# Performance work log

Measured on AMD Instinct MI355X. Metric: run time of the kernel, lower is better.

The kernel has to match this reference:

```python
import jax, jax.numpy as jnp
import numpy as np

D_MODEL = 1024
D_STATE = 64
BATCH = 16
SEQ = 4096


def setup_inputs() -> dict:
    key = jax.random.key(0)
    ks = jax.random.split(key, 4)
    x = jax.random.normal(ks[0], (BATCH, SEQ, D_MODEL), dtype=jnp.float32)
    A = jax.random.normal(ks[1], (D_STATE, D_STATE), dtype=jnp.float32) * 0.01
    B_mat = jax.random.normal(ks[2], (D_STATE, D_MODEL), dtype=jnp.float32) * 0.01
    C = jax.random.normal(ks[3], (D_MODEL, D_STATE), dtype=jnp.float32) * 0.01
    gamma = jnp.ones((D_MODEL,), dtype=jnp.float32)
    beta = jnp.zeros((D_MODEL,), dtype=jnp.float32)
    return {"x": x, "A": A, "B_mat": B_mat, "C": C, "gamma": gamma, "beta": beta}


def reference(x, A, B_mat, C, gamma, beta):
    # x: [B, L, D]; linear SSM recurrence: s_t = s_{t-1} A^T + u_t B^T, y_t = s_t C^T
    Bsz = x.shape[0]
    xu = jnp.einsum('bld,sd->lbs', x, B_mat)  # precompute input projection [L, B, S]

    def step(state, u_t):
        state = state @ A.T + u_t          # [B, S]
        return state, state

    init = jnp.zeros((Bsz, D_STATE), dtype=x.dtype)
    _, states = jax.lax.scan(step, init, xu)   # [L, B, S]
    y = jnp.einsum('lbs,ds->bld', states, C)   # [B, L, D]

    act = jax.nn.gelu(y, approximate=False)    # torch nn.GELU default = exact
    mean = jnp.mean(act, axis=-1, keepdims=True)
    var = jnp.var(act, axis=-1, keepdims=True)
    normed = (act - mean) * jax.lax.rsqrt(var + 1e-5) * gamma + beta
    return jnp.nan_to_num(normed, nan=0.0, posinf=1e6, neginf=-1e6)
```

## Files before the change

### kernel.cpp

```cpp
#include <hip/hip_runtime.h>
#include <hip/hip_bf16.h>
#include <math.h>

#define BSZ  16
#define LSEQ 4096
#define DM   1024
#define DS   64
#define CHK  64
#define NCHK 64
#define FK   12
#define FIXT 8

typedef __bf16 bf16;
typedef bf16  bf16x8 __attribute__((ext_vector_type(8)));
typedef bf16  bf16x4 __attribute__((ext_vector_type(4)));
typedef float f32x4  __attribute__((ext_vector_type(4)));

#define MFMA(a,b,c) __builtin_amdgcn_mfma_f32_16x16x32_bf16((a),(b),(c),0,0,0)

__global__ __launch_bounds__(256) void k_prep(const float* __restrict__ Bm,
                                              const float* __restrict__ Cm,
                                              bf16* __restrict__ Bh,
                                              bf16* __restrict__ Ch) {
    int i = blockIdx.x * 256 + threadIdx.x;
    Bh[i] = (bf16)Bm[i];
    Ch[i] = (bf16)Cm[i];
}

__global__ __launch_bounds__(1024) void k_apow(const float* __restrict__ A,
                                               bf16* __restrict__ Apow) {
    __shared__ float P0[64 * 64], P1[64 * 64];
    const int tid = threadIdx.x;
    const int i = tid >> 4, j4 = (tid & 15) * 4;

    #pragma unroll
    for (int q = 0; q < 4; ++q) {
        int j = j4 + q;
        Apow[i * 64 + j] = (bf16)((i == j) ? 1.f : 0.f);
        P0[i * 64 + j]   = A[i * 64 + j];
    }
    __syncthreads();

    float* cur = P0; float* nxt = P1;
    for (int k = 1; k < FK; ++k) {
        const float4 v = *(const float4*)&cur[i * 64 + j4];
        Apow[k * 4096 + i * 64 + j4 + 0] = (bf16)v.x;
        Apow[k * 4096 + i * 64 + j4 + 1] = (bf16)v.y;
        Apow[k * 4096 + i * 64 + j4 + 2] = (bf16)v.z;
        Apow[k * 4096 + i * 64 + j4 + 3] = (bf16)v.w;
        float a0 = 0.f, a1 = 0.f, a2 = 0.f, a3 = 0.f;
        for (int m = 0; m < 64; ++m) {
            const float am = A[i * 64 + m];
            const float4 cr = *(const float4*)&cur[m * 64 + j4];
            a0 = fmaf(am, cr.x, a0);
            a1 = fmaf(am, cr.y, a1);
            a2 = fmaf(am, cr.z, a2);
            a3 = fmaf(am, cr.w, a3);
        }
        __syncthreads();
        nxt[i * 64 + j4 + 0] = a0;
        nxt[i * 64 + j4 + 1] = a1;
        nxt[i * 64 + j4 + 2] = a2;
        nxt[i * 64 + j4 + 3] = a3;
        __syncthreads();
        float* t = cur; cur = nxt; nxt = t;
    }
}

__global__ __launch_bounds__(256) void k_fir(const float* __restrict__ x,
                                             const bf16* __restrict__ Bh,
                                             const bf16* __restrict__ Apow,
                                             bf16* __restrict__ states) {
    const int c = blockIdx.x, b = blockIdx.y;
    const int tid = threadIdx.x, lane = tid & 63, w = tid >> 6;
    const int fr = lane & 15;
    const int kg = (lane >> 4) * 8;
    const int rg = (lane >> 4) * 4;

    __shared__ __align__(16) bf16 ulds[76][72];
    __shared__ __align__(16) bf16 slds[64][72];

    if (tid < 216) *(float2*)((char*)ulds + tid * 8) = make_float2(0.f, 0.f);

    const float* xrow  = x  + (size_t)(b * LSEQ + c * CHK + w * 16 + fr) * DM + kg;
    const bf16*  bbase = Bh + (size_t)fr * DM + kg;

    f32x4 acc[4] = {};
    #pragma unroll 4
    for (int ks = 0; ks < 1024; ks += 32) {
        float4 lo = *(const float4*)(xrow + ks);
        float4 hi = *(const float4*)(xrow + ks + 4);
        bf16x8 af = {(bf16)lo.x, (bf16)lo.y, (bf16)lo.z, (bf16)lo.w,
                     (bf16)hi.x, (bf16)hi.y, (bf16)hi.z, (bf16)hi.w};
        #pragma unroll
        for (int nt = 0; nt < 4; ++nt) {
            bf16x8 bf = *(const bf16x8*)(bbase + (size_t)nt * 16 * DM + ks);
            acc[nt] = MFMA(af, bf, acc[nt]);
        }
    }

    #pragma unroll
    for (int nt = 0; nt < 4; ++nt)
        #pragma unroll
        for (int q = 0; q < 4; ++q)
            ulds[12 + w * 16 + rg + q][nt * 16 + fr] = (bf16)acc[nt][q];
    __syncthreads();

    const bf16* apb = Apow + (size_t)fr * DS + kg;
    f32x4 acc2[4] = {};
    #pragma unroll
    for (int k = 0; k < FK; ++k) {
        const int r0 = 12 + w * 16 - k;
        bf16x8 a0 = *(const bf16x8*)&ulds[r0 + fr][kg];
        bf16x8 a1 = *(const bf16x8*)&ulds[r0 + fr][32 + kg];
        #pragma unroll
        for (int nt = 0; nt < 4; ++nt) {
            bf16x8 b0 = *(const bf16x8*)(apb + (size_t)k * 4096 + nt * 16 * DS);
            bf16x8 b1 = *(const bf16x8*)(apb + (size_t)k * 4096 + nt * 16 * DS + 32);
            acc2[nt] = MFMA(a0, b0, acc2[nt]);
            acc2[nt] = MFMA(a1, b1, acc2[nt]);
        }
    }

    #pragma unroll
    for (int nt = 0; nt < 4; ++nt)
        #pragma unroll
        for (int q = 0; q < 4; ++q)
            slds[w * 16 + rg + q][nt * 16 + fr] = (bf16)acc2[nt][q];
    __syncthreads();

    const int r  = tid >> 2;
    const int c0 = (tid & 3) * 16;
    bf16x8 s0 = *(const bf16x8*)&slds[r][c0];
    bf16x8 s1 = *(const bf16x8*)&slds[r][c0 + 8];
    bf16* sp = states + (size_t)(b * LSEQ + c * CHK + r) * DS + c0;
    *(bf16x8*)sp       = s0;
    *(bf16x8*)(sp + 8) = s1;
}

__device__ __forceinline__ float scan_step(const float* a, float s, float u) {
    float p0 = u, p1 = 0.f, p2 = 0.f, p3 = 0.f;
    #pragma unroll
    for (int j = 0; j < 64; j += 4) {
        p0 = fmaf(a[j + 0], __shfl(s, j + 0), p0);
        p1 = fmaf(a[j + 1], __shfl(s, j + 1), p1);
        p2 = fmaf(a[j + 2], __shfl(s, j + 2), p2);
        p3 = fmaf(a[j + 3], __shfl(s, j + 3), p3);
    }
    return (p0 + p1) + (p2 + p3);
}

__global__ __launch_bounds__(64) void k_fix(const float* __restrict__ A,
                                            bf16* __restrict__ states) {
    const int c = blockIdx.x + 1, b = blockIdx.y, lane = threadIdx.x;
    float a[64];
    #pragma unroll
    for (int j4 = 0; j4 < 16; ++j4) {
        float4 v = *(const float4*)&A[lane * 64 + j4 * 4];
        a[j4*4+0] = v.x; a[j4*4+1] = v.y; a[j4*4+2] = v.z; a[j4*4+3] = v.w;
    }
    float v = (float)states[(size_t)(b * LSEQ + c * CHK - 1) * DS + lane];
    bf16* sp = states + (size_t)(b * LSEQ + c * CHK) * DS + lane;
    #pragma unroll
    for (int t = 0; t < FIXT; ++t) {
        v = scan_step(a, v, 0.f);
        float snew = (float)sp[t * DS] + v;
        sp[t * DS] = (bf16)snew;
    }
}

__global__ __launch_bounds__(256) void k_out(const bf16* __restrict__ st,
                                             const bf16* __restrict__ Ch,
                                             const float* __restrict__ gamma,
                                             const float* __restrict__ beta,
                                             float* __restrict__ out) {
    const int R = blockIdx.x * 16;
    const int tid = threadIdx.x, lane = tid & 63, wave = tid >> 6;
    const int fr = lane & 15;
    const int kg = (lane >> 4) * 8;
    const int rg = (lane >> 4) * 4;

    __shared__ bf16  act[64 * 16 * 16];
    __shared__ float redS[4][16], redQ[4][16];
    __shared__ float meanL[16], rstdL[16];

    bf16x8 b0 = *(const bf16x8*)&st[(size_t)(R + fr) * DS + kg];
    bf16x8 b1 = *(const bf16x8*)&st[(size_t)(R + fr) * DS + 32 + kg];

    float sum = 0.f, sq = 0.f;
    const int nbase = wave * 256;

    #pragma unroll
    for (int nt = 0; nt < 16; ++nt) {
        const int d0 = nbase + nt * 16 + fr;
        bf16x8 a0 = *(const bf16x8*)&Ch[(size_t)d0 * DS + kg];
        bf16x8 a1 = *(const bf16x8*)&Ch[(size_t)d0 * DS + 32 + kg];
        f32x4 t = (f32x4){0.f, 0.f, 0.f, 0.f};
        t = MFMA(a0, b0, t);
        t = MFMA(a1, b1, t);

        bf16x4 av;
        #pragma unroll
        for (int q = 0; q < 4; ++q) {
            float v = t[q];
            float g = 0.5f * v * (1.f + erff(v * 0.70710678118654752f));
            sum += g; sq += g * g;
            av[q] = (bf16)g;
        }
        const int ntg = wave * 16 + nt;
        int byte = ntg * 512 + fr * 32 + rg * 2;
        byte ^= (ntg & 7) << 4;
        *(bf16x4*)((char*)act + byte) = av;
    }

    sum += __shfl_xor(sum, 16); sq += __shfl_xor(sq, 16);
    sum += __shfl_xor(sum, 32); sq += __shfl_xor(sq, 32);
    if (lane < 16) { redS[wave][fr] = sum; redQ[wave][fr] = sq; }
    __syncthreads();

    if (tid < 16) {
        float S = redS[0][tid] + redS[1][tid] + redS[2][tid] + redS[3][tid];
        float Q = redQ[0][tid] + redQ[1][tid] + redQ[2][tid] + redQ[3][tid];
        float mu  = S * (1.f / 1024.f);
        float var = Q * (1.f / 1024.f) - mu * mu;
        meanL[tid] = mu;
        rstdL[tid] = rsqrtf(var + 1e-5f);
    }
    __syncthreads();

    #pragma unroll
    for (int rr = 0; rr < 4; ++rr) {
        const int r = wave * 4 + rr;
        const float mu = meanL[r], rs = rstdL[r];
        #pragma unroll
        for (int half = 0; half < 2; ++half) {
            const int d = half * 512 + lane * 8;
            const int ntg = d >> 4;
            int byte = ntg * 512 + r * 32 + (lane & 1) * 16;
            byte ^= (ntg & 7) << 4;
            bf16x8 av = *(const bf16x8*)((char*)act + byte);

            float4 g0  = *(const float4*)&gamma[d];
            float4 g1  = *(const float4*)&gamma[d + 4];
            float4 be0 = *(const float4*)&beta[d];
            float4 be1 = *(const float4*)&beta[d + 4];
            float4 o0, o1;
            o0.x = ((float)av[0] - mu) * rs * g0.x + be0.x;
            o0.y = ((float)av[1] - mu) * rs * g0.y + be0.y;
            o0.z = ((float)av[2] - mu) * rs * g0.z + be0.z;
            o0.w = ((float)av[3] - mu) * rs * g0.w + be0.w;
            o1.x = ((float)av[4] - mu) * rs * g1.x + be1.x;
            o1.y = ((float)av[5] - mu) * rs * g1.y + be1.y;
            o1.z = ((float)av[6] - mu) * rs * g1.z + be1.z;
            o1.w = ((float)av[7] - mu) * rs * g1.w + be1.w;

            float* orow = out + (size_t)(R + r) * DM + d;
            *(float4*)orow       = o0;
            *(float4*)(orow + 4) = o1;
        }
    }
}

extern "C" void kernel_launch(void* const* d_in, const int* in_sizes, int n_in,
                              void* d_out, int out_size, void* d_ws, size_t ws_size,
                              hipStream_t stream) {
    (void)in_sizes; (void)n_in; (void)out_size; (void)ws_size;
    const float* x     = (const float*)d_in[0];
    const float* A     = (const float*)d_in[1];
    const float* Bm    = (const float*)d_in[2];
    const float* Cm    = (const float*)d_in[3];
    const float* gamma = (const float*)d_in[4];
    const float* beta  = (const float*)d_in[5];
    float* out = (float*)d_out;

    char* ws = (char*)d_ws;
    bf16* states = (bf16*)(ws);
    bf16* Bh     = (bf16*)(ws + 8388608);
    bf16* Ch     = (bf16*)(ws + 8519680);
    bf16* Apow   = (bf16*)(ws + 8650752);

    k_prep<<<dim3(256),           dim3(256),  0, stream>>>(Bm, Cm, Bh, Ch);
    k_apow<<<dim3(1),             dim3(1024), 0, stream>>>(A, Apow);
    k_fir <<<dim3(NCHK, BSZ),     dim3(256),  0, stream>>>(x, Bh, Apow, states);
    k_fix <<<dim3(NCHK - 1, BSZ), dim3(64),   0, stream>>>(A, states);
    k_out <<<dim3(4096),          dim3(256),  0, stream>>>(states, Ch, gamma, beta, out);
}
```

Before: 297.9 us.

## Stage x and B tiles through LDS in FIR projection; pad A-power LDS

The input-projection GEMM in k_fir now loads 128-wide K tiles of x (converted to bf16) and B into shared memory with coalesced row-contiguous loads, then feeds the MFMAs from LDS. Before, each lane read strided fragments straight from global memory. The shared buffers are aliased with the later ulds/slds arrays to keep LDS usage the same. The change aims to improve global load coalescing and reuse B across waves. In exchange it adds two barriers per K tile with no double buffering, and it uses a 130-element row stride that leaves vector LDS accesses only 4-byte aligned. k_apow also caches A in LDS and pads its matrices to a stride of 65 to avoid bank conflicts.

After: 499.8 us. 67.8% more time.

```diff
diff --git a/kernel.cpp b/kernel.cpp
--- a/kernel.cpp
+++ b/kernel.cpp
@@ -10,6 +10,7 @@
 #define NCHK 64
 #define FK   12
 #define FIXT 8
+#define BK   128
 
 typedef __bf16 bf16;
 typedef bf16  bf16x8 __attribute__((ext_vector_type(8)));
@@ -29,39 +30,38 @@
 
 __global__ __launch_bounds__(1024) void k_apow(const float* __restrict__ A,
                                                bf16* __restrict__ Apow) {
-    __shared__ float P0[64 * 64], P1[64 * 64];
+    __shared__ float aA[64 * 65], P0[64 * 65], P1[64 * 65];
     const int tid = threadIdx.x;
     const int i = tid >> 4, j4 = (tid & 15) * 4;
 
     #pragma unroll
     for (int q = 0; q < 4; ++q) {
-        int j = j4 + q;
-        Apow[i * 64 + j] = (bf16)((i == j) ? 1.f : 0.f);
-        P0[i * 64 + j]   = A[i * 64 + j];
+        float v = A[i * 64 + j4 + q];
+        aA[i * 65 + j4 + q] = v;
+        P0[i * 65 + j4 + q] = v;
+        Apow[i * 64 + j4 + q] = (bf16)((i == j4 + q) ? 1.f : 0.f);
     }
     __syncthreads();
 
     float* cur = P0; float* nxt = P1;
     for (int k = 1; k < FK; ++k) {
-        const float4 v = *(const float4*)&cur[i * 64 + j4];
-        Apow[k * 4096 + i * 64 + j4 + 0] = (bf16)v.x;
-        Apow[k * 4096 + i * 64 + j4 + 1] = (bf16)v.y;
-        Apow[k * 4096 + i * 64 + j4 + 2] = (bf16)v.z;
-        Apow[k * 4096 + i * 64 + j4 + 3] = (bf16)v.w;
+        #pragma unroll
+        for (int q = 0; q < 4; ++q)
+            Apow[k * 4096 + i * 64 + j4 + q] = (bf16)cur[i * 65 + j4 + q];
         float a0 = 0.f, a1 = 0.f, a2 = 0.f, a3 = 0.f;
         for (int m = 0; m < 64; ++m) {
-            const float am = A[i * 64 + m];
-            const float4 cr = *(const float4*)&cur[m * 64 + j4];
+            const float am = aA[i * 65 + m];
+            const float4 cr = *(const float4*)&cur[m * 65 + j4];
             a0 = fmaf(am, cr.x, a0);
             a1 = fmaf(am, cr.y, a1);
             a2 = fmaf(am, cr.z, a2);
             a3 = fmaf(am, cr.w, a3);
         }
         __syncthreads();
-        nxt[i * 64 + j4 + 0] = a0;
-        nxt[i * 64 + j4 + 1] = a1;
-        nxt[i * 64 + j4 + 2] = a2;
-        nxt[i * 64 + j4 + 3] = a3;
+        nxt[i * 65 + j4 + 0] = a0;
+        nxt[i * 65 + j4 + 1] = a1;
+        nxt[i * 65 + j4 + 2] = a2;
+        nxt[i * 65 + j4 + 3] = a3;
         __syncthreads();
         float* t = cur; cur = nxt; nxt = t;
     }
@@ -77,28 +77,48 @@
     const int kg = (lane >> 4) * 8;
     const int rg = (lane >> 4) * 4;
 
-    __shared__ __align__(16) bf16 ulds[76][72];
-    __shared__ __align__(16) bf16 slds[64][72];
+    __shared__ __align__(16) char smem[33280];
+    bf16 (*xs)[130] = (bf16(*)[130])(smem);
+    bf16 (*bs)[130] = (bf16(*)[130])(smem + 16640);
+    bf16 (*ulds)[72] = (bf16(*)[72])(smem);
+    bf16 (*slds)[72] = (bf16(*)[72])(smem + 16640);
+
+    const int r2 = lane >> 5;
+    const int cf = (lane & 31) * 4;
+    const int r4 = lane >> 4;
+    const int cb = (lane & 15) * 8;
+
+    const size_t xbase = (size_t)(b * LSEQ + c * CHK) * DM;
+
+    f32x4 acc[4] = {};
+    for (int kb = 0; kb < DM; kb += BK) {
+        #pragma unroll
+        for (int i = 0; i < 8; ++i) {
+            const int row = w * 16 + i * 2 + r2;
+            float4 v = *(const float4*)(x + xbase + (size_t)row * DM + kb + cf);
+            bf16x4 h = {(bf16)v.x, (bf16)v.y, (bf16)v.z, (bf16)v.w};
+            *(bf16x4*)&xs[row][cf] = h;
+        }
+        #pragma unroll
+        for (int i = 0; i < 4; ++i) {
+            const int row = w * 16 + i * 4 + r4;
+            bf16x8 v = *(const bf16x8*)(Bh + (size_t)row * DM + kb + cb);
+            *(bf16x8*)&bs[row][cb] = v;
+        }
+        __syncthreads();
+        #pragma unroll
+        for (int ks = 0; ks < BK; ks += 32) {
+            bf16x8 af = *(const bf16x8*)&xs[w * 16 + fr][ks + kg];
+            #pragma unroll
+            for (int nt = 0; nt < 4; ++nt) {
+                bf16x8 bf = *(const bf16x8*)&bs[nt * 16 + fr][ks + kg];
+                acc[nt] = MFMA(af, bf, acc[nt]);
+            }
+        }
+        __syncthreads();
+    }
 
     if (tid < 216) *(float2*)((char*)ulds + tid * 8) = make_float2(0.f, 0.f);
-
-    const float* xrow  = x  + (size_t)(b * LSEQ + c * CHK + w * 16 + fr) * DM + kg;
-    const bf16*  bbase = Bh + (size_t)fr * DM + kg;
-
-    f32x4 acc[4] = {};
-    #pragma unroll 4
-    for (int ks = 0; ks < 1024; ks += 32) {
-        float4 lo = *(const float4*)(xrow + ks);
-        float4 hi = *(const float4*)(xrow + ks + 4);
-        bf16x8 af = {(bf16)lo.x, (bf16)lo.y, (bf16)lo.z, (bf16)lo.w,
-                     (bf16)hi.x, (bf16)hi.y, (bf16)hi.z, (bf16)hi.w};
-        #pragma unroll
-        for (int nt = 0; nt < 4; ++nt) {
-            bf16x8 bf = *(const bf16x8*)(bbase + (size_t)nt * 16 * DM + ks);
-            acc[nt] = MFMA(af, bf, acc[nt]);
-        }
-    }
-
     #pragma unroll
     for (int nt = 0; nt < 4; ++nt)
         #pragma unroll
```
